# Optimization experiments

Measured on AMD Instinct MI355X. Metric: run time of the kernel, lower is better.

## Reference

```python
import jax, jax.numpy as jnp
import numpy as np

UNI, HID, FLD = 512, 1024, 128
B, S = 128, 512

def setup_inputs() -> dict:
    key = jax.random.key(0)
    ks = jax.random.split(key, 8)
    input_embeddings = jax.random.normal(ks[0], (B, S, UNI), dtype=jnp.float32)
    field_embeddings = jax.random.normal(ks[1], (B, S, FLD), dtype=jnp.float32)
    input_length = jax.random.randint(ks[2], (B,), 1, S + 1)
    input_length = input_length.at[0].set(S)  # ensure loop runs full S steps -> static output shape
    s1 = 1.0 / np.sqrt(UNI + HID)
    s2 = 1.0 / np.sqrt(FLD)
    W1 = jax.random.uniform(ks[3], (4 * HID, UNI + HID), minval=-s1, maxval=s1, dtype=jnp.float32)
    b1 = jax.random.uniform(ks[4], (4 * HID,), minval=-s1, maxval=s1, dtype=jnp.float32)
    W2 = jax.random.uniform(ks[5], (2 * HID, FLD), minval=-s2, maxval=s2, dtype=jnp.float32)
    b2 = jax.random.uniform(ks[6], (2 * HID,), minval=-s2, maxval=s2, dtype=jnp.float32)
    return {"input_embeddings": input_embeddings, "field_embeddings": field_embeddings,
            "input_length": input_length, "W1": W1, "b1": b1, "W2": W2, "b2": b2}

def reference(input_embeddings, field_embeddings, input_length, W1, b1, W2, b2):
    Bc, Sc, _ = input_embeddings.shape
    H = W1.shape[0] // 4
    h0 = jnp.zeros((Bc, H), dtype=input_embeddings.dtype)
    c0 = jnp.zeros((Bc, H), dtype=input_embeddings.dtype)

    def step(carry, xs):
        h_prev, c_prev, t = carry
        x_t, f_t = xs
        fin = (t >= input_length)[:, None]  # [B,1] bool
        pre = jnp.concatenate([x_t, h_prev], axis=1) @ W1.T + b1  # [B,4H]
        i, j, f, o = jnp.split(pre, 4, axis=1)
        rd = f_t @ W2.T + b2  # [B,2H]
        r, d = jnp.split(rd, 2, axis=1)
        c = (jax.nn.sigmoid(f + 1.0) * c_prev
             + jax.nn.sigmoid(i) * jnp.tanh(j)
             + jax.nn.sigmoid(r) * jnp.tanh(d))
        h = jax.nn.sigmoid(o) * jnp.tanh(c)
        out = jnp.where(fin, 0.0, h)
        h_new = jnp.where(fin, h_prev, h)
        c_new = jnp.where(fin, c_prev, c)
        return (h_new, c_new, t + 1), out

    xs = (input_embeddings.transpose(1, 0, 2), field_embeddings.transpose(1, 0, 2))
    (h, c, _), outs = jax.lax.scan(step, (h0, c0, jnp.int32(0)), xs)
    return outs.transpose(1, 0, 2), (h, c)
```

## Files before the change

kernel.cpp:

```cpp
#include <hip/hip_runtime.h>
#include <cstdint>
#include <cstddef>


typedef __bf16 bf16;
typedef __bf16 bf16x8 __attribute__((ext_vector_type(8)));
typedef float floatx4 __attribute__((ext_vector_type(4)));

#define B_ 128
#define S_ 512
#define UNI_ 512
#define HID_ 1024
#define FLD_ 128
#define K1_ 1536
#define BS_STRIDE 1544

__device__ __forceinline__ float sigf(float x) { return 1.0f / (1.0f + __expf(-x)); }

__global__ __launch_bounds__(128) void sort_kernel(const int* __restrict__ len,
                                                   int* __restrict__ perm,
                                                   int* __restrict__ lens) {
  int i = threadIdx.x;
  int li = len[i];
  int r = 0;
  for (int j = 0; j < B_; ++j) {
    int lj = len[j];
    r += (lj > li) || (lj == li && j < i) ? 1 : 0;
  }
  perm[r] = i;
  lens[r] = li;
}

__global__ __launch_bounds__(256) void conv_w(const float* __restrict__ W1,
                                              const float* __restrict__ W2,
                                              bf16* __restrict__ W1b,
                                              bf16* __restrict__ W2b) {
  int i = blockIdx.x * 256 + threadIdx.x;
  if (i < 4096 * K1_) W1b[i] = (bf16)W1[i];
  else {
    int j = i - 4096 * K1_;
    if (j < 2048 * FLD_) W2b[j] = (bf16)W2[j];
  }
}

__global__ __launch_bounds__(256) void zero_state(bf16* __restrict__ h0,
                                                  bf16* __restrict__ h1,
                                                  float* __restrict__ c,
                                                  float* __restrict__ hf) {
  int i = blockIdx.x * 256 + threadIdx.x;
  h0[i] = (bf16)0.0f;
  h1[i] = (bf16)0.0f;
  c[i] = 0.0f;
  hf[i] = 0.0f;
}

__global__ __launch_bounds__(256) void conv_xf(const float* __restrict__ x,
                                               const float* __restrict__ f,
                                               const int* __restrict__ perm,
                                               bf16* __restrict__ xbf,
                                               bf16* __restrict__ fbf) {
  int t = blockIdx.x, rs = blockIdx.y, tid = threadIdx.x;
  int b = perm[rs];
  const float* xs = x + ((size_t)b * S_ + t) * UNI_;
  bf16* xd = xbf + ((size_t)rs * S_ + t) * UNI_;
  xd[tid] = (bf16)xs[tid];
  xd[tid + 256] = (bf16)xs[tid + 256];
  if (tid < FLD_) {
    fbf[((size_t)rs * S_ + t) * FLD_ + tid] =
        (bf16)f[((size_t)b * S_ + t) * FLD_ + tid];
  }
}

__global__ __launch_bounds__(256) void zero_tail(const int* __restrict__ len,
                                                 float* __restrict__ out) {
  int t = blockIdx.x, b = blockIdx.y;
  if (t < len[b]) return;
  float4 z = {0.0f, 0.0f, 0.0f, 0.0f};
  float4* o = (float4*)(out + ((size_t)b * S_ + t) * HID_);
  o[threadIdx.x] = z;
}

__global__ __launch_bounds__(512, 2) void step_kernel(
    const bf16* __restrict__ xbf,
    const bf16* __restrict__ fbf,
    const bf16* __restrict__ W1b,
    const bf16* __restrict__ W2b,
    const float* __restrict__ bias1,
    const float* __restrict__ bias2,
    const bf16* __restrict__ h_cur,
    bf16* __restrict__ h_nxt,
    float* __restrict__ c_ws,
    float* __restrict__ hf,
    const int* __restrict__ perm_g,
    const int* __restrict__ lens_g,
    float* __restrict__ out, int t) {
  __shared__ bf16 Bs[16 * BS_STRIDE];
  __shared__ float pre_s[128][17];
  __shared__ float rd_s[128][9];
  __shared__ int lens_s[128];
  __shared__ int perm_s[128];

  const int tid = threadIdx.x;
  const int nb = blockIdx.x;
  const int c0 = nb * 4;

  {
    const int n = tid >> 5;
    const int s = tid & 31;
    const int wrow = (n >> 2) * HID_ + c0 + (n & 3);
    const bf16* src = W1b + (size_t)wrow * K1_;
    bf16* dst = Bs + n * BS_STRIDE;
#pragma unroll
    for (int p = 0; p < 6; ++p) {
      int off = (p * 32 + s) * 8;
      *(bf16x8*)(dst + off) = *(const bf16x8*)(src + off);
    }
  }
  if (tid < 128) {
    lens_s[tid] = lens_g[tid];
    perm_s[tid] = perm_g[tid];
  }
  __syncthreads();

  const int wave = tid >> 6;
  const int lane = tid & 63;
  const int quad = lane >> 4;
  const int l16 = lane & 15;
  const int m = wave * 16 + l16;
  const int kq = quad * 8;

  const bool wave_active = (t < lens_s[wave * 16]);

  if (wave_active) {
    floatx4 acc_a = {0.f, 0.f, 0.f, 0.f};
    floatx4 acc_b = {0.f, 0.f, 0.f, 0.f};
    floatx4 accr = {0.f, 0.f, 0.f, 0.f};
    const bf16* xrow = xbf + ((size_t)m * S_ + t) * UNI_ + kq;
    const bf16* hrow = h_cur + (size_t)m * HID_ + kq;
    const bf16* bsl = Bs + l16 * BS_STRIDE + kq;

#pragma unroll
    for (int kc = 0; kc < UNI_; kc += 64) {
      bf16x8 a0 = *(const bf16x8*)(xrow + kc);
      bf16x8 b0 = *(const bf16x8*)(bsl + kc);
      bf16x8 a1 = *(const bf16x8*)(xrow + kc + 32);
      bf16x8 b1 = *(const bf16x8*)(bsl + kc + 32);
      acc_a = __builtin_amdgcn_mfma_f32_16x16x32_bf16(a0, b0, acc_a, 0, 0, 0);
      acc_b = __builtin_amdgcn_mfma_f32_16x16x32_bf16(a1, b1, acc_b, 0, 0, 0);
    }
#pragma unroll 8
    for (int kc = 0; kc < HID_; kc += 64) {
      bf16x8 a0 = *(const bf16x8*)(hrow + kc);
      bf16x8 b0 = *(const bf16x8*)(bsl + UNI_ + kc);
      bf16x8 a1 = *(const bf16x8*)(hrow + kc + 32);
      bf16x8 b1 = *(const bf16x8*)(bsl + UNI_ + kc + 32);
      acc_a = __builtin_amdgcn_mfma_f32_16x16x32_bf16(a0, b0, acc_a, 0, 0, 0);
      acc_b = __builtin_amdgcn_mfma_f32_16x16x32_bf16(a1, b1, acc_b, 0, 0, 0);
    }
    {
      const bf16* frow = fbf + ((size_t)m * S_ + t) * FLD_ + kq;
      const int w2row = ((l16 >> 2) & 1) * HID_ + c0 + (l16 & 3);
      const bf16* w2p = W2b + (size_t)w2row * FLD_ + kq;
#pragma unroll
      for (int kc = 0; kc < FLD_; kc += 32) {
        bf16x8 a0 = *(const bf16x8*)(frow + kc);
        bf16x8 b0 = *(const bf16x8*)(w2p + kc);
        accr = __builtin_amdgcn_mfma_f32_16x16x32_bf16(a0, b0, accr, 0, 0, 0);
      }
    }
    const int row0 = wave * 16 + quad * 4;
#pragma unroll
    for (int r = 0; r < 4; ++r) {
      pre_s[row0 + r][l16] = acc_a[r] + acc_b[r];
      if (l16 < 8) rd_s[row0 + r][l16] = accr[r];
    }
  }
  __syncthreads();

  {
    const int row = tid >> 2;
    const int cc = tid & 3;
    const int col = c0 + cc;
    const size_t sidx = (size_t)row * HID_ + col;
    if (t >= lens_s[row]) {
      h_nxt[sidx] = h_cur[sidx];
    } else {
      float iv = pre_s[row][cc] + bias1[col];
      float jv = pre_s[row][4 + cc] + bias1[HID_ + col];
      float fv = pre_s[row][8 + cc] + bias1[2 * HID_ + col];
      float ov = pre_s[row][12 + cc] + bias1[3 * HID_ + col];
      float rv = rd_s[row][cc] + bias2[col];
      float dv = rd_s[row][4 + cc] + bias2[HID_ + col];
      float cp = c_ws[sidx];
      float cn = sigf(fv + 1.0f) * cp + sigf(iv) * tanhf(jv) + sigf(rv) * tanhf(dv);
      float hn = sigf(ov) * tanhf(cn);
      out[(size_t)perm_s[row] * (S_ * HID_) + (size_t)t * HID_ + col] = hn;
      h_nxt[sidx] = (bf16)hn;
      c_ws[sidx] = cn;
      hf[sidx] = hn;
    }
  }
}

__global__ __launch_bounds__(256) void final_kernel(const float* __restrict__ hf,
                                                    const float* __restrict__ c,
                                                    const int* __restrict__ perm,
                                                    float* __restrict__ out) {
  int i = blockIdx.x * 256 + threadIdx.x;
  int rs = i >> 10, n = i & 1023;
  int b = perm[rs];
  const size_t base = (size_t)B_ * S_ * HID_;
  out[base + (size_t)b * HID_ + n] = hf[i];
  out[base + (size_t)B_ * HID_ + (size_t)b * HID_ + n] = c[i];
}

extern "C" void kernel_launch(void* const* d_in, const int* in_sizes, int n_in,
                              void* d_out, int out_size, void* d_ws, size_t ws_size,
                              hipStream_t stream) {
  const float* x = (const float*)d_in[0];
  const float* f = (const float*)d_in[1];
  const int* len = (const int*)d_in[2];
  const float* W1 = (const float*)d_in[3];
  const float* b1 = (const float*)d_in[4];
  const float* W2 = (const float*)d_in[5];
  const float* b2 = (const float*)d_in[6];
  float* out = (float*)d_out;

  char* ws = (char*)d_ws;
  bf16* W1b = (bf16*)(ws);
  bf16* W2b = (bf16*)(ws + 12582912);
  bf16* xbf = (bf16*)(ws + 13107200);
  bf16* fbf = (bf16*)(ws + 80216064);
  bf16* h0 = (bf16*)(ws + 96993280);
  bf16* h1 = (bf16*)(ws + 97255424);
  float* c = (float*)(ws + 97517568);
  float* hf = (float*)(ws + 98041856);
  int* perm = (int*)(ws + 98566144);
  int* lens = (int*)(ws + 98566656);

  sort_kernel<<<1, 128, 0, stream>>>(len, perm, lens);
  conv_w<<<(4096 * K1_ + 2048 * FLD_ + 255) / 256, 256, 0, stream>>>(W1, W2, W1b, W2b);
  zero_state<<<512, 256, 0, stream>>>(h0, h1, c, hf);
  conv_xf<<<dim3(S_, B_), 256, 0, stream>>>(x, f, perm, xbf, fbf);
  zero_tail<<<dim3(S_, B_), 256, 0, stream>>>(len, out);

  for (int t = 0; t < S_; ++t) {
    const bf16* hc = (t & 1) ? h1 : h0;
    bf16* hn = (t & 1) ? h0 : h1;
    step_kernel<<<256, 512, 0, stream>>>(xbf, fbf, W1b, W2b, b1, b2, hc, hn, c,
                                         hf, perm, lens, out, t);
  }

  final_kernel<<<512, 256, 0, stream>>>(hf, c, perm, out);
}
```

Measured before the change: 7.862 ms.

## Replace per-timestep kernel launches with persistent kernel and global barrier

Runs the 512 recurrent steps inside one persistent kernel of 256 blocks and replaces the per-step launches with a device-wide barrier: block 0 polls per-block done counters, then publishes a go flag. The W1 hidden-part slice, W2 slice and biases stay resident in LDS for the whole kernel. The input and field projections for step t+1 are computed before the barrier wait so they overlap it. This removes launch overhead and the repeated weight reloads, but relies on all 256 blocks being co-resident and adds spin-wait latency through a single coordinating block.

```diff
diff --git a/kernel.cpp b/kernel.cpp
--- a/kernel.cpp
+++ b/kernel.cpp
@@ -13,7 +13,9 @@
 #define HID_ 1024
 #define FLD_ 128
 #define K1_ 1536
-#define BS_STRIDE 1544
+#define NB_ 256
+#define W1S_STRIDE 1032
+#define W2S_STRIDE 136
 
 __device__ __forceinline__ float sigf(float x) { return 1.0f / (1.0f + __expf(-x)); }
 
@@ -46,12 +48,16 @@
 __global__ __launch_bounds__(256) void zero_state(bf16* __restrict__ h0,
                                                   bf16* __restrict__ h1,
                                                   float* __restrict__ c,
-                                                  float* __restrict__ hf) {
+                                                  float* __restrict__ hf,
+                                                  int* __restrict__ done,
+                                                  int* __restrict__ go) {
   int i = blockIdx.x * 256 + threadIdx.x;
   h0[i] = (bf16)0.0f;
   h1[i] = (bf16)0.0f;
   c[i] = 0.0f;
   hf[i] = 0.0f;
+  if (i < NB_) done[i] = 0;
+  if (i == NB_) *go = 0;
 }
 
 __global__ __launch_bounds__(256) void conv_xf(const float* __restrict__ x,
@@ -80,138 +86,193 @@
   o[threadIdx.x] = z;
 }
 
-__global__ __launch_bounds__(512, 2) void step_kernel(
+__global__ __launch_bounds__(512, 2) void persist_kernel(
     const bf16* __restrict__ xbf,
     const bf16* __restrict__ fbf,
     const bf16* __restrict__ W1b,
     const bf16* __restrict__ W2b,
-    const float* __restrict__ bias1,
-    const float* __restrict__ bias2,
-    const bf16* __restrict__ h_cur,
-    bf16* __restrict__ h_nxt,
-    float* __restrict__ c_ws,
-    float* __restrict__ hf,
-    const int* __restrict__ perm_g,
-    const int* __restrict__ lens_g,
-    float* __restrict__ out, int t) {
-  __shared__ bf16 Bs[16 * BS_STRIDE];
+    const float* __restrict__ bias1, const float* __restrict__ bias2,
+    bf16* __restrict__ hbuf0, bf16* __restrict__ hbuf1,
+    float* __restrict__ c_ws, float* __restrict__ hf,
+    const int* __restrict__ perm_g, const int* __restrict__ lens_g,
+    int* __restrict__ done, int* __restrict__ go,
+    float* __restrict__ out) {
+  __shared__ bf16 W1s[16 * W1S_STRIDE];
+  __shared__ bf16 W2s[8 * W2S_STRIDE];
   __shared__ float pre_s[128][17];
   __shared__ float rd_s[128][9];
   __shared__ int lens_s[128];
   __shared__ int perm_s[128];
+  __shared__ float b1_s[16];
+  __shared__ float b2_s[8];
 
   const int tid = threadIdx.x;
-  const int nb = blockIdx.x;
-  const int c0 = nb * 4;
+  const int bid = blockIdx.x;
+  const int c0 = bid * 4;
 
   {
-    const int n = tid >> 5;
-    const int s = tid & 31;
-    const int wrow = (n >> 2) * HID_ + c0 + (n & 3);
-    const bf16* src = W1b + (size_t)wrow * K1_;
-    bf16* dst = Bs + n * BS_STRIDE;
-#pragma unroll
-    for (int p = 0; p < 6; ++p) {
-      int off = (p * 32 + s) * 8;
-      *(bf16x8*)(dst + off) = *(const bf16x8*)(src + off);
-    }
+    int nl = tid >> 5;
+    int sg = tid & 31;
+    int w1row = (nl >> 2) * HID_ + c0 + (nl & 3);
+    const bf16* src = W1b + (size_t)w1row * K1_ + UNI_ + sg * 32;
+    bf16* dst = W1s + nl * W1S_STRIDE + sg * 32;
+#pragma unroll
+    for (int p = 0; p < 4; ++p)
+      *(bf16x8*)(dst + p * 8) = *(const bf16x8*)(src + p * 8);
   }
   if (tid < 128) {
-    lens_s[tid] = lens_g[tid];
-    perm_s[tid] = perm_g[tid];
-  }
+    int nl = tid >> 4, sg = tid & 15;
+    int w2row = (nl >> 2) * HID_ + c0 + (nl & 3);
+    *(bf16x8*)(W2s + nl * W2S_STRIDE + sg * 8) =
+        *(const bf16x8*)(W2b + (size_t)w2row * FLD_ + sg * 8);
+  }
+  if (tid < 128) { lens_s[tid] = lens_g[tid]; perm_s[tid] = perm_g[tid]; }
+  if (tid < 16) b1_s[tid] = bias1[(tid >> 2) * HID_ + c0 + (tid & 3)];
+  if (tid < 8) b2_s[tid] = bias2[(tid >> 2) * HID_ + c0 + (tid & 3)];
   __syncthreads();
 
   const int wave = tid >> 6;
   const int lane = tid & 63;
   const int quad = lane >> 4;
   const int l16 = lane & 15;
+  const int kq = quad * 8;
   const int m = wave * 16 + l16;
-  const int kq = quad * 8;
-
-  const bool wave_active = (t < lens_s[wave * 16]);
-
-  if (wave_active) {
-    floatx4 acc_a = {0.f, 0.f, 0.f, 0.f};
-    floatx4 acc_b = {0.f, 0.f, 0.f, 0.f};
-    floatx4 accr = {0.f, 0.f, 0.f, 0.f};
-    const bf16* xrow = xbf + ((size_t)m * S_ + t) * UNI_ + kq;
-    const bf16* hrow = h_cur + (size_t)m * HID_ + kq;
-    const bf16* bsl = Bs + l16 * BS_STRIDE + kq;
-
-#pragma unroll
-    for (int kc = 0; kc < UNI_; kc += 64) {
-      bf16x8 a0 = *(const bf16x8*)(xrow + kc);
-      bf16x8 b0 = *(const bf16x8*)(bsl + kc);
-      bf16x8 a1 = *(const bf16x8*)(xrow + kc + 32);
-      bf16x8 b1 = *(const bf16x8*)(bsl + kc + 32);
-      acc_a = __builtin_amdgcn_mfma_f32_16x16x32_bf16(a0, b0, acc_a, 0, 0, 0);
-      acc_b = __builtin_amdgcn_mfma_f32_16x16x32_bf16(a1, b1, acc_b, 0, 0, 0);
-    }
+  const int mylen = lens_s[wave * 16];
+
+  const int w1row = (l16 >> 2) * HID_ + c0 + (l16 & 3);
+  const bf16* w1x = W1b + (size_t)w1row * K1_ + kq;
+  const bf16* w1h = W1s + l16 * W1S_STRIDE + kq;
+  const bf16* w2l = W2s + (l16 & 7) * W2S_STRIDE + kq;
+  const bf16* xrow = xbf + (size_t)m * S_ * UNI_ + kq;
+  const bf16* frow = fbf + (size_t)m * S_ * FLD_ + kq;
+
+  floatx4 acc = {0.f, 0.f, 0.f, 0.f};
+  floatx4 rdacc = {0.f, 0.f, 0.f, 0.f};
+
+  {
+    const bf16* xr = xrow;
+#pragma unroll
+    for (int ki = 0; ki < 16; ++ki) {
+      bf16x8 a = *(const bf16x8*)(xr + 32 * ki);
+      bf16x8 b = *(const bf16x8*)(w1x + 32 * ki);
+      acc = __builtin_amdgcn_mfma_f32_16x16x32_bf16(a, b, acc, 0, 0, 0);
+    }
+#pragma unroll
+    for (int ki = 0; ki < 4; ++ki) {
+      bf16x8 a = *(const bf16x8*)(frow + 32 * ki);
+      bf16x8 b = *(const bf16x8*)(w2l + 32 * ki);
+      rdacc = __builtin_amdgcn_mfma_f32_16x16x32_bf16(a, b, rdacc, 0, 0, 0);
+    }
+  }
+
+  for (int t = 0; t < S_; ++t) {
+    const bf16* h_cur = (t & 1) ? hbuf1 : hbuf0;
+    bf16* h_nxt = (t & 1) ? hbuf0 : hbuf1;
+
+    if (t > 0) {
+      if (bid == 0) {
+        if (tid < NB_) {
+          while (__hip_atomic_load(&done[tid], __ATOMIC_RELAXED,
+                                   __HIP_MEMORY_SCOPE_AGENT) < t)
+            __builtin_amdgcn_s_sleep(1);
+        }
+        __syncthreads();
+        if (tid == 0) {
+          __builtin_amdgcn_fence(__ATOMIC_ACQ_REL, "agent");
+          __hip_atomic_store(go, t, __ATOMIC_RELAXED, __HIP_MEMORY_SCOPE_AGENT);
+        }
+      } else {
+        if (tid == 0) {
+          while (__hip_atomic_load(go, __ATOMIC_RELAXED,
+                                   __HIP_MEMORY_SCOPE_AGENT) < t)
+            __builtin_amdgcn_s_sleep(1);
+          __builtin_amdgcn_fence(__ATOMIC_ACQUIRE, "agent");
+        }
+      }
+      __syncthreads();
+    }
+
+    const bool act = (t < mylen);
+
+    if (act) {
+      const bf16* hr = h_cur + (size_t)m * HID_ + kq;
 #pragma unroll 8
-    for (int kc = 0; kc < HID_; kc += 64) {
-      bf16x8 a0 = *(const bf16x8*)(hrow + kc);
-      bf16x8 b0 = *(const bf16x8*)(bsl + UNI_ + kc);
-      bf16x8 a1 = *(const bf16x8*)(hrow + kc + 32);
-      bf16x8 b1 = *(const bf16x8*)(bsl + UNI_ + kc + 32);
-      acc_a = __builtin_amdgcn_mfma_f32_16x16x32_bf16(a0, b0, acc_a, 0, 0, 0);
-      acc_b = __builtin_amdgcn_mfma_f32_16x16x32_bf16(a1, b1, acc_b, 0, 0, 0);
-    }
+      for (int ki = 0; ki < 32; ++ki) {
+        bf16x8 a = *(const bf16x8*)(hr + 32 * ki);
+        bf16x8 b = *(const bf16x8*)(w1h + 32 * ki);
+        acc = __builtin_amdgcn_mfma_f32_16x16x32_bf16(a, b, acc, 0, 0, 0);
+      }
+      const int row0 = wave * 16 + quad * 4;
+#pragma unroll
+      for (int r = 0; r < 4; ++r) {
+        pre_s[row0 + r][l16] = acc[r];
+        if (l16 < 8) rd_s[row0 + r][l16] = rdacc[r];
+      }
+    }
+    __syncthreads();
+
     {
-      const bf16* frow = fbf + ((size_t)m * S_ + t) * FLD_ + kq;
-      const int w2row = ((l16 >> 2) & 1) * HID_ + c0 + (l16 & 3);
-      const bf16* w2p = W2b + (size_t)w2row * FLD_ + kq;
-#pragma unroll
-      for (int kc = 0; kc < FLD_; kc += 32) {
-        bf16x8 a0 = *(const bf16x8*)(frow + kc);
-        bf16x8 b0 = *(const bf16x8*)(w2p + kc);
-        accr = __builtin_amdgcn_mfma_f32_16x16x32_bf16(a0, b0, accr, 0, 0, 0);
-      }
-    }
-    const int row0 = wave * 16 + quad * 4;
-#pragma unroll
-    for (int r = 0; r < 4; ++r) {
-      pre_s[row0 + r][l16] = acc_a[r] + acc_b[r];
-      if (l16 < 8) rd_s[row0 + r][l16] = accr[r];
-    }
-  }
-  __syncthreads();
+      const int row = tid >> 2;
+      const int cc = tid & 3;
+      const int col = c0 + cc;
+      const size_t sidx = (size_t)row * HID_ + col;
+      if (t >= lens_s[row]) {
+        h_nxt[sidx] = h_cur[sidx];
+      } else {
+        float iv = pre_s[row][cc] + b1_s[cc];
+        float jv = pre_s[row][4 + cc] + b1_s[4 + cc];
+        float fv = pre_s[row][8 + cc] + b1_s[8 + cc];
+        float ov = pre_s[row][12 + cc] + b1_s[12 + cc];
+        float rv = rd_s[row][cc] + b2_s[cc];
+        float dv = rd_s[row][4 + cc] + b2_s[4 + cc];
+        float cp = c_ws[sidx];
+        float cn = sigf(fv + 1.0f) * cp + sigf(iv) * tanhf(jv) + sigf(rv) * tanhf(dv);
+        float hn = sigf(ov) * tanhf(cn);
+        out[(size_t)perm_s[row] * (S_ * HID_) + (size_t)t * HID_ + col] = hn;
+        h_nxt[sidx] = (bf16)hn;
+        c_ws[sidx] = cn;
+        hf[sidx] = hn;
+      }
+    }
+    __syncthreads();
+
+    if (tid == 0) {
+      __builtin_amdgcn_fence(__ATOMIC_RELEASE, "agent");
+      __hip_atomic_store(&done[bid], t + 1, __ATOMIC_RELAXED,
+                         __HIP_MEMORY_SCOPE_AGENT);
+    }
+
+    if (t + 1 < S_) {
+      acc = (floatx4){0.f, 0.f, 0.f, 0.f};
+      rdacc = (floatx4){0.f, 0.f, 0.f, 0.f};
+      if (t + 1 < mylen) {
+        const bf16* xr = xrow + (size_t)(t + 1) * UNI_;
+#pragma unroll
+        for (int ki = 0; ki < 16; ++ki) {
+          bf16x8 a = *(const bf16x8*)(xr + 32 * ki);
+          bf16x8 b = *(const bf16x8*)(w1x + 32 * ki);
+          acc = __builtin_amdgcn_mfma_f32_16x16x32_bf16(a, b, acc, 0, 0, 0);
+        }
+        const bf16* fr = frow + (size_t)(t + 1) * FLD_;
+#pragma unroll
+        for (int ki = 0; ki < 4; ++ki) {
+          bf16x8 a = *(const bf16x8*)(fr + 32 * ki);
+          bf16x8 b = *(const bf16x8*)(w2l + 32 * ki);
+          rdacc = __builtin_amdgcn_mfma_f32_16x16x32_bf16(a, b, rdacc, 0, 0, 0);
+        }
+      }
+    }
+  }
 
   {
     const int row = tid >> 2;
-    const int cc = tid & 3;
-    const int col = c0 + cc;
+    const int col = c0 + (tid & 3);
     const size_t sidx = (size_t)row * HID_ + col;
-    if (t >= lens_s[row]) {
-      h_nxt[sidx] = h_cur[sidx];
-    } else {
-      float iv = pre_s[row][cc] + bias1[col];
-      float jv = pre_s[row][4 + cc] + bias1[HID_ + col];
-      float fv = pre_s[row][8 + cc] + bias1[2 * HID_ + col];
-      float ov = pre_s[row][12 + cc] + bias1[3 * HID_ + col];
-      float rv = rd_s[row][cc] + bias2[col];
-      float dv = rd_s[row][4 + cc] + bias2[HID_ + col];
-      float cp = c_ws[sidx];
-      float cn = sigf(fv + 1.0f) * cp + sigf(iv) * tanhf(jv) + sigf(rv) * tanhf(dv);
-      float hn = sigf(ov) * tanhf(cn);
-      out[(size_t)perm_s[row] * (S_ * HID_) + (size_t)t * HID_ + col] = hn;
-      h_nxt[sidx] = (bf16)hn;
-      c_ws[sidx] = cn;
-      hf[sidx] = hn;
-    }
-  }
-}
-
-__global__ __launch_bounds__(256) void final_kernel(const float* __restrict__ hf,
-                                                    const float* __restrict__ c,
-                                                    const int* __restrict__ perm,
-                                                    float* __restrict__ out) {
-  int i = blockIdx.x * 256 + threadIdx.x;
-  int rs = i >> 10, n = i & 1023;
-  int b = perm[rs];
-  const size_t base = (size_t)B_ * S_ * HID_;
-  out[base + (size_t)b * HID_ + n] = hf[i];
-  out[base + (size_t)B_ * HID_ + (size_t)b * HID_ + n] = c[i];
+    const size_t baseH = (size_t)B_ * S_ * HID_;
+    const size_t baseC = baseH + (size_t)B_ * HID_;
+    out[baseH + (size_t)perm_s[row] * HID_ + col] = hf[sidx];
+    out[baseC + (size_t)perm_s[row] * HID_ + col] = c_ws[sidx];
+  }
 }
 
 extern "C" void kernel_launch(void* const* d_in, const int* in_sizes, int n_in,
@@ -237,19 +298,15 @@
   float* hf = (float*)(ws + 98041856);
   int* perm = (int*)(ws + 98566144);
   int* lens = (int*)(ws + 98566656);
+  int* done = (int*)(ws + 98567168);
+  int* go = (int*)(ws + 98568192);
 
   sort_kernel<<<1, 128, 0, stream>>>(len, perm, lens);
   conv_w<<<(4096 * K1_ + 2048 * FLD_ + 255) / 256, 256, 0, stream>>>(W1, W2, W1b, W2b);
-  zero_state<<<512, 256, 0, stream>>>(h0, h1, c, hf);
+  zero_state<<<512, 256, 0, stream>>>(h0, h1, c, hf, done, go);
   conv_xf<<<dim3(S_, B_), 256, 0, stream>>>(x, f, perm, xbf, fbf);
   zero_tail<<<dim3(S_, B_), 256, 0, stream>>>(len, out);
 
-  for (int t = 0; t < S_; ++t) {
-    const bf16* hc = (t & 1) ? h1 : h0;
-    bf16* hn = (t & 1) ? h0 : h1;
-    step_kernel<<<256, 512, 0, stream>>>(xbf, fbf, W1b, W2b, b1, b2, hc, hn, c,
-                                         hf, perm, lens, out, t);
-  }
-
-  final_kernel<<<512, 256, 0, stream>>>(hf, c, perm, out);
-}
+  persist_kernel<<<NB_, 512, 0, stream>>>(xbf, fbf, W1b, W2b, b1, b2, h0, h1, c,
+                                          hf, perm, lens, done, go, out);
+}
```

After: 10.41 ms. 1.32x slower.
